# Kernel tuning notes

Measured on AMD Instinct MI355X. Metric: run time of the kernel, lower is better.

Reference implementation:

```python
import jax, jax.numpy as jnp
import numpy as np

B, V, C, H, W, D = 2, 3, 8, 128, 160, 64


def bilinear_sample(feat, grid):
    """feat: [B,C,H,W]; grid: [B,N,2] normalized to [-1,1], align_corners=True,
    padding_mode='zeros' (matches F.grid_sample). Returns [B,C,N]."""
    b, c, h, w = feat.shape
    ix = (grid[..., 0] + 1.0) * 0.5 * (w - 1)  # [B,N]
    iy = (grid[..., 1] + 1.0) * 0.5 * (h - 1)
    x0 = jnp.floor(ix)
    y0 = jnp.floor(iy)
    wx1 = ix - x0
    wy1 = iy - y0
    flat = feat.reshape(b, c, h * w)

    def corner(xi, yi, wgt):
        valid = (xi >= 0) & (xi <= w - 1) & (yi >= 0) & (yi <= h - 1)
        xc = jnp.clip(xi, 0, w - 1).astype(jnp.int32)
        yc = jnp.clip(yi, 0, h - 1).astype(jnp.int32)
        idx = yc * w + xc  # [B,N]
        vals = jnp.take_along_axis(flat, jnp.broadcast_to(idx[:, None, :], (b, c, idx.shape[1])), axis=2)
        return vals * (wgt * valid.astype(feat.dtype))[:, None, :]

    out = (corner(x0, y0, (1 - wx1) * (1 - wy1))
           + corner(x0 + 1, y0, wx1 * (1 - wy1))
           + corner(x0, y0 + 1, (1 - wx1) * wy1)
           + corner(x0 + 1, y0 + 1, wx1 * wy1))
    return out


def homo_warping(src_feat, proj_mat, depth_values):
    """src_feat [B,C,H,W], proj_mat [B,3,4], depth_values [B,D,H,W].
    Returns warped volume [B,C,D,H,W] and normalized grid [B,D,H,W,2]."""
    b, c, h, w = src_feat.shape
    d = depth_values.shape[1]
    R = proj_mat[:, :, :3]
    T = proj_mat[:, :, 3:]  # [B,3,1]
    ys, xs = jnp.meshgrid(jnp.arange(h, dtype=src_feat.dtype),
                          jnp.arange(w, dtype=src_feat.dtype), indexing='ij')
    ref = jnp.stack([xs.ravel(), ys.ravel(), jnp.ones(h * w, src_feat.dtype)], 0)  # [3,HW]
    Rp = jnp.einsum('bij,jp->bip', R, ref)  # [B,3,HW]
    dv = depth_values.reshape(b, d, h * w)
    src = Rp[:, :, None, :] + T[:, :, :, None] / dv[:, None, :, :]  # [B,3,D,HW]
    xy = src[:, :2] / src[:, 2:3]
    gx = xy[:, 0] / ((w - 1) / 2.0) - 1.0
    gy = xy[:, 1] / ((h - 1) / 2.0) - 1.0
    grid = jnp.stack([gx, gy], axis=-1)  # [B,D,HW,2]
    warped = bilinear_sample(src_feat, grid.reshape(b, d * h * w, 2)).reshape(b, c, d, h, w)
    return warped, grid.reshape(b, d, h, w, 2)


def setup_inputs() -> dict:
    key = jax.random.key(0)
    k1, k2, k3, k4, k5 = jax.random.split(key, 5)
    features = jax.random.normal(k1, (V, B, C, H, W), dtype=jnp.float32)
    # near-identity projective maps so warps land mostly in-bounds
    eye = jnp.broadcast_to(jnp.eye(3, dtype=jnp.float32), (B, V, 3, 3))
    Rm = eye + 0.01 * jax.random.normal(k2, (B, V, 3, 3), dtype=jnp.float32)
    Tm = 2.0 * jax.random.normal(k3, (B, V, 3, 1), dtype=jnp.float32)
    proj_matrices = jnp.concatenate([Rm, Tm], axis=-1)  # [B,V,3,4]
    base = jnp.linspace(2.0, 10.0, D, dtype=jnp.float32)[None, :, None, None]
    depth_values = base + 0.1 * jax.random.uniform(k4, (B, D, H, W), dtype=jnp.float32)
    reg_weight = jax.random.normal(k5, (C,), dtype=jnp.float32)
    return {"features": features, "proj_matrices": proj_matrices,
            "depth_values": depth_values, "reg_weight": reg_weight,
            "num_depth": D}


def reference(features, proj_matrices, depth_values, reg_weight, num_depth):
    v = features.shape[0]
    ref_feat = features[0]
    b, c, h, w = ref_feat.shape
    d = num_depth
    ref_volume = jnp.broadcast_to(ref_feat[:, :, None], (b, c, d, h, w))
    volume_sum = ref_volume
    volume_sq_sum = ref_volume ** 2
    in_masks = jnp.ones((b, 1, d, h, w), dtype=ref_feat.dtype)
    for i in range(1, v):  # fixed small number of source views
        warped, grid = homo_warping(features[i], proj_matrices[:, i], depth_values)
        m = (grid > -1.0) & (grid < 1.0)
        in_masks = in_masks + (m[..., 0] & m[..., 1]).astype(ref_feat.dtype)[:, None]
        volume_sum = volume_sum + warped
        volume_sq_sum = volume_sq_sum + warped ** 2
    count = 1.0 / in_masks
    volume_feat = volume_sq_sum * count - (volume_sum * count) ** 2  # [B,C,D,H,W]
    # stand-in cost regularization: channel reduction -> [B,D,H,W]
    cost = jnp.einsum('bcdhw,c->bdhw', volume_feat, reg_weight)
    prob_volume = jax.nn.softmax(cost, axis=1)
    depth = jnp.sum(prob_volume * depth_values, axis=1)  # [B,H,W]
    return depth
```

## Files before the change

### kernel.cpp

```cpp
#include <hip/hip_runtime.h>
#include <math.h>

#define BB 2
#define VV 3
#define CC 8
#define HH 128
#define WW 160
#define DD 64
constexpr int HW = HH * WW;
constexpr int NPIX = BB * HW;
constexpr int PX_PER_BLOCK = 16;
constexpr int CHUNKS = 16;
constexpr int DEPTHS_PER_CHUNK = DD / CHUNKS;

__global__ __launch_bounds__(256)
void transpose_feats(const float* __restrict__ feats, float* __restrict__ ft)
{
    const int t = blockIdx.x * blockDim.x + threadIdx.x;
    if (t >= VV * BB * HW) return;
    const int vb = t / HW;
    const int hw = t - vb * HW;
    const float* src = feats + (size_t)vb * CC * HW + hw;
    float* dst = ft + (size_t)vb * HW * CC + (size_t)hw * CC;
    float4 lo, hi;
    lo.x = src[0 * HW]; lo.y = src[1 * HW]; lo.z = src[2 * HW]; lo.w = src[3 * HW];
    hi.x = src[4 * HW]; hi.y = src[5 * HW]; hi.z = src[6 * HW]; hi.w = src[7 * HW];
    ((float4*)dst)[0] = lo;
    ((float4*)dst)[1] = hi;
}

__global__ __launch_bounds__(256)
void depthnet_fused(const float* __restrict__ ft,
                    const float* __restrict__ proj,
                    const float* __restrict__ depthv,
                    const float* __restrict__ regw,
                    float* __restrict__ out)
{
    __shared__ float sm_m[4 * PX_PER_BLOCK];
    __shared__ float sm_l[4 * PX_PER_BLOCK];
    __shared__ float sm_s[4 * PX_PER_BLOCK];

    const int tid   = threadIdx.x;
    const int lane  = tid & 63;
    const int wave  = tid >> 6;
    const int px    = lane & 15;
    const int sub   = lane >> 4;
    const int chunk = wave * 4 + sub;
    const int pixel = blockIdx.x * PX_PER_BLOCK + px;

    const int b  = (pixel >= HW) ? 1 : 0;
    const int hw = pixel - b * HW;
    const int h  = hw / WW;
    const int w  = hw - h * WW;

    const float* f0 = ft + ((size_t)b * HW + hw) * CC;
    float rf[CC], rf2[CC];
    {
        float4 lo = ((const float4*)f0)[0];
        float4 hi = ((const float4*)f0)[1];
        rf[0] = lo.x; rf[1] = lo.y; rf[2] = lo.z; rf[3] = lo.w;
        rf[4] = hi.x; rf[5] = hi.y; rf[6] = hi.z; rf[7] = hi.w;
    }
#pragma unroll
    for (int c = 0; c < CC; ++c) rf2[c] = rf[c] * rf[c];

    float Rp[2][3], Tv[2][3];
    const float xf = (float)w, yf = (float)h;
#pragma unroll
    for (int v = 0; v < 2; ++v) {
        const float* M = proj + ((size_t)b * VV + (v + 1)) * 12;
#pragma unroll
        for (int i = 0; i < 3; ++i) {
            Rp[v][i] = M[i * 4 + 0] * xf + M[i * 4 + 1] * yf + M[i * 4 + 2];
            Tv[v][i] = M[i * 4 + 3];
        }
    }

    const float* fsrc0 = ft + ((size_t)(1 * BB + b)) * HW * CC;
    const float* fsrc1 = ft + ((size_t)(2 * BB + b)) * HW * CC;

    float m = -INFINITY, l = 0.f, s = 0.f;

    const float* dvp = depthv + (size_t)b * DD * HW + hw;
    const int d0 = chunk * DEPTHS_PER_CHUNK;

    for (int dd = 0; dd < DEPTHS_PER_CHUNK; ++dd) {
        const int d = d0 + dd;
        const float dv = dvp[(size_t)d * HW];
        const float inv_dv = __builtin_amdgcn_rcpf(dv);

        float sum[CC], sq[CC];
#pragma unroll
        for (int c = 0; c < CC; ++c) { sum[c] = rf[c]; sq[c] = rf2[c]; }
        float nmask = 1.0f;

#pragma unroll
        for (int v = 0; v < 2; ++v) {
            const float* fb = (v == 0) ? fsrc0 : fsrc1;
            const float sx = Rp[v][0] + Tv[v][0] * inv_dv;
            const float sy = Rp[v][1] + Tv[v][1] * inv_dv;
            const float sz = Rp[v][2] + Tv[v][2] * inv_dv;
            const float rsz = __builtin_amdgcn_rcpf(sz);
            const float ix = sx * rsz;
            const float iy = sy * rsz;
            nmask += ((ix > 0.f) && (ix < (float)(WW - 1)) &&
                      (iy > 0.f) && (iy < (float)(HH - 1))) ? 1.0f : 0.0f;
            const float x0f = floorf(ix), y0f = floorf(iy);
            const float wx1 = ix - x0f, wy1 = iy - y0f;
            const float wx0 = 1.f - wx1, wy0 = 1.f - wy1;
            const float x1f = x0f + 1.f, y1f = y0f + 1.f;
            const bool vx0 = (x0f >= 0.f) && (x0f <= (float)(WW - 1));
            const bool vx1 = (x1f >= 0.f) && (x1f <= (float)(WW - 1));
            const bool vy0 = (y0f >= 0.f) && (y0f <= (float)(HH - 1));
            const bool vy1 = (y1f >= 0.f) && (y1f <= (float)(HH - 1));
            const float w00 = wx0 * wy0 * ((vx0 && vy0) ? 1.f : 0.f);
            const float w01 = wx1 * wy0 * ((vx1 && vy0) ? 1.f : 0.f);
            const float w10 = wx0 * wy1 * ((vx0 && vy1) ? 1.f : 0.f);
            const float w11 = wx1 * wy1 * ((vx1 && vy1) ? 1.f : 0.f);
            const int x0c = (int)fminf(fmaxf(x0f, 0.f), (float)(WW - 1));
            const int x1c = (int)fminf(fmaxf(x1f, 0.f), (float)(WW - 1));
            const int y0c = (int)fminf(fmaxf(y0f, 0.f), (float)(HH - 1));
            const int y1c = (int)fminf(fmaxf(y1f, 0.f), (float)(HH - 1));
            const int i00 = (y0c * WW + x0c) * CC;
            const int i01 = (y0c * WW + x1c) * CC;
            const int i10 = (y1c * WW + x0c) * CC;
            const int i11 = (y1c * WW + x1c) * CC;

            float val[CC];
            {
                float4 lo = *(const float4*)(fb + i00);
                float4 hi = *(const float4*)(fb + i00 + 4);
                val[0] = lo.x * w00; val[1] = lo.y * w00; val[2] = lo.z * w00; val[3] = lo.w * w00;
                val[4] = hi.x * w00; val[5] = hi.y * w00; val[6] = hi.z * w00; val[7] = hi.w * w00;
            }
            {
                float4 lo = *(const float4*)(fb + i01);
                float4 hi = *(const float4*)(fb + i01 + 4);
                val[0] += lo.x * w01; val[1] += lo.y * w01; val[2] += lo.z * w01; val[3] += lo.w * w01;
                val[4] += hi.x * w01; val[5] += hi.y * w01; val[6] += hi.z * w01; val[7] += hi.w * w01;
            }
            {
                float4 lo = *(const float4*)(fb + i10);
                float4 hi = *(const float4*)(fb + i10 + 4);
                val[0] += lo.x * w10; val[1] += lo.y * w10; val[2] += lo.z * w10; val[3] += lo.w * w10;
                val[4] += hi.x * w10; val[5] += hi.y * w10; val[6] += hi.z * w10; val[7] += hi.w * w10;
            }
            {
                float4 lo = *(const float4*)(fb + i11);
                float4 hi = *(const float4*)(fb + i11 + 4);
                val[0] += lo.x * w11; val[1] += lo.y * w11; val[2] += lo.z * w11; val[3] += lo.w * w11;
                val[4] += hi.x * w11; val[5] += hi.y * w11; val[6] += hi.z * w11; val[7] += hi.w * w11;
            }

#pragma unroll
            for (int c = 0; c < CC; ++c) {
                sum[c] += val[c];
                sq[c]  += val[c] * val[c];
            }
        }

        const float cnt = __builtin_amdgcn_rcpf(nmask);
        float t1 = 0.f, t2 = 0.f;
#pragma unroll
        for (int c = 0; c < CC; ++c) {
            t1 += regw[c] * sq[c];
            t2 += (regw[c] * sum[c]) * sum[c];
        }
        const float cost = cnt * t1 - (cnt * cnt) * t2;

        const float M = fmaxf(m, cost);
        const float e_old = __expf(m - M);
        const float e_new = __expf(cost - M);
        l = l * e_old + e_new;
        s = s * e_old + e_new * dv;
        m = M;
    }

#pragma unroll
    for (int off = 16; off < 64; off <<= 1) {
        const float m2 = __shfl_xor(m, off, 64);
        const float l2 = __shfl_xor(l, off, 64);
        const float s2 = __shfl_xor(s, off, 64);
        const float M  = fmaxf(m, m2);
        const float e1 = __expf(m - M);
        const float e2 = __expf(m2 - M);
        l = l * e1 + l2 * e2;
        s = s * e1 + s2 * e2;
        m = M;
    }

    if (lane < PX_PER_BLOCK) {
        sm_m[wave * PX_PER_BLOCK + px] = m;
        sm_l[wave * PX_PER_BLOCK + px] = l;
        sm_s[wave * PX_PER_BLOCK + px] = s;
    }
    __syncthreads();

    if (tid < PX_PER_BLOCK) {
        float M = sm_m[tid], L = sm_l[tid], S = sm_s[tid];
#pragma unroll
        for (int wv = 1; wv < 4; ++wv) {
            const float m2 = sm_m[wv * PX_PER_BLOCK + tid];
            const float l2 = sm_l[wv * PX_PER_BLOCK + tid];
            const float s2 = sm_s[wv * PX_PER_BLOCK + tid];
            const float Mn = fmaxf(M, m2);
            const float e1 = __expf(M - Mn);
            const float e2 = __expf(m2 - Mn);
            L = L * e1 + l2 * e2;
            S = S * e1 + s2 * e2;
            M = Mn;
        }
        out[blockIdx.x * PX_PER_BLOCK + tid] = S / L;
    }
}

extern "C" void kernel_launch(void* const* d_in, const int* in_sizes, int n_in,
                              void* d_out, int out_size, void* d_ws, size_t ws_size,
                              hipStream_t stream) {
    const float* feats  = (const float*)d_in[0];
    const float* proj   = (const float*)d_in[1];
    const float* depthv = (const float*)d_in[2];
    const float* regw   = (const float*)d_in[3];
    float* out = (float*)d_out;
    float* ft  = (float*)d_ws;

    {
        const int n = VV * BB * HW;
        const int block = 256;
        const int grid = (n + block - 1) / block;
        hipLaunchKernelGGL(transpose_feats, dim3(grid), dim3(block), 0, stream,
                           feats, ft);
    }
    {
        const int grid = NPIX / PX_PER_BLOCK;
        hipLaunchKernelGGL(depthnet_fused, dim3(grid), dim3(256), 0, stream,
                           ft, proj, depthv, regw, out);
    }
}
```

Measured before the change: 105.2 us.

## Transpose depth values, batch gather loads, and swizzle blocks across XCDs

Adds a kernel that transposes depth values to a pixel-major [B,HW,D] layout, so each thread reads its four depths with one float4 load instead of four strided loads. Hoists all 16 bilinear corner loads for both source views ahead of the arithmetic to raise memory-level parallelism. Remaps block indices so each XCD handles a contiguous pixel range, aiming for better L2 locality. The cost is an extra kernel launch, an extra full pass over the depth tensor, and more live registers.

```diff
diff --git a/kernel.cpp b/kernel.cpp
--- a/kernel.cpp
+++ b/kernel.cpp
@@ -12,6 +12,8 @@
 constexpr int PX_PER_BLOCK = 16;
 constexpr int CHUNKS = 16;
 constexpr int DEPTHS_PER_CHUNK = DD / CHUNKS;
+constexpr int GRID_FUSED = NPIX / PX_PER_BLOCK;
+constexpr int XCD_STRIDE = GRID_FUSED / 8;
 
 __global__ __launch_bounds__(256)
 void transpose_feats(const float* __restrict__ feats, float* __restrict__ ft)
@@ -30,9 +32,42 @@
 }
 
 __global__ __launch_bounds__(256)
+void transpose_dv(const float* __restrict__ dv, float* __restrict__ dvT)
+{
+    __shared__ float tile[64 * 65];
+    const int t   = threadIdx.x;
+    const int blk = blockIdx.x;
+    const int b   = blk / (HW / 64);
+    const int hw0 = (blk % (HW / 64)) * 64;
+
+    const float* src = dv + (size_t)b * DD * HW + hw0;
+    const int px = t & 63;
+    const int dq = t >> 6;
+#pragma unroll
+    for (int j = 0; j < 16; ++j) {
+        const int d = dq * 16 + j;
+        tile[px * 65 + d] = src[(size_t)d * HW + px];
+    }
+    __syncthreads();
+
+    float* dst = dvT + ((size_t)b * HW + hw0) * DD;
+    const int c = t & 15;
+#pragma unroll
+    for (int j = 0; j < 4; ++j) {
+        const int p = (t >> 4) + j * 16;
+        float4 v;
+        v.x = tile[p * 65 + c * 4 + 0];
+        v.y = tile[p * 65 + c * 4 + 1];
+        v.z = tile[p * 65 + c * 4 + 2];
+        v.w = tile[p * 65 + c * 4 + 3];
+        ((float4*)(dst + (size_t)p * DD))[c] = v;
+    }
+}
+
+__global__ __launch_bounds__(256)
 void depthnet_fused(const float* __restrict__ ft,
                     const float* __restrict__ proj,
-                    const float* __restrict__ depthv,
+                    const float* __restrict__ dvT,
                     const float* __restrict__ regw,
                     float* __restrict__ out)
 {
@@ -46,7 +81,8 @@
     const int px    = lane & 15;
     const int sub   = lane >> 4;
     const int chunk = wave * 4 + sub;
-    const int pixel = blockIdx.x * PX_PER_BLOCK + px;
+    const int bswz  = (blockIdx.x & 7) * XCD_STRIDE + (blockIdx.x >> 3);
+    const int pixel = bswz * PX_PER_BLOCK + px;
 
     const int b  = (pixel >= HW) ? 1 : 0;
     const int hw = pixel - b * HW;
@@ -79,24 +115,23 @@
     const float* fsrc0 = ft + ((size_t)(1 * BB + b)) * HW * CC;
     const float* fsrc1 = ft + ((size_t)(2 * BB + b)) * HW * CC;
 
+    const float4 dv4 = *(const float4*)(dvT + ((size_t)b * HW + hw) * DD + chunk * 4);
+    float dvv[4] = {dv4.x, dv4.y, dv4.z, dv4.w};
+    float inv[4];
+#pragma unroll
+    for (int k = 0; k < 4; ++k) inv[k] = __builtin_amdgcn_rcpf(dvv[k]);
+
     float m = -INFINITY, l = 0.f, s = 0.f;
 
-    const float* dvp = depthv + (size_t)b * DD * HW + hw;
-    const int d0 = chunk * DEPTHS_PER_CHUNK;
-
     for (int dd = 0; dd < DEPTHS_PER_CHUNK; ++dd) {
-        const int d = d0 + dd;
-        const float dv = dvp[(size_t)d * HW];
-        const float inv_dv = __builtin_amdgcn_rcpf(dv);
-
-        float sum[CC], sq[CC];
-#pragma unroll
-        for (int c = 0; c < CC; ++c) { sum[c] = rf[c]; sq[c] = rf2[c]; }
+        const float dv = dvv[dd];
+        const float inv_dv = inv[dd];
+
+        float wt[2][4];
+        int   ib[2][4];
         float nmask = 1.0f;
-
 #pragma unroll
         for (int v = 0; v < 2; ++v) {
-            const float* fb = (v == 0) ? fsrc0 : fsrc1;
             const float sx = Rp[v][0] + Tv[v][0] * inv_dv;
             const float sy = Rp[v][1] + Tv[v][1] * inv_dv;
             const float sz = Rp[v][2] + Tv[v][2] * inv_dv;
@@ -113,50 +148,63 @@
             const bool vx1 = (x1f >= 0.f) && (x1f <= (float)(WW - 1));
             const bool vy0 = (y0f >= 0.f) && (y0f <= (float)(HH - 1));
             const bool vy1 = (y1f >= 0.f) && (y1f <= (float)(HH - 1));
-            const float w00 = wx0 * wy0 * ((vx0 && vy0) ? 1.f : 0.f);
-            const float w01 = wx1 * wy0 * ((vx1 && vy0) ? 1.f : 0.f);
-            const float w10 = wx0 * wy1 * ((vx0 && vy1) ? 1.f : 0.f);
-            const float w11 = wx1 * wy1 * ((vx1 && vy1) ? 1.f : 0.f);
+            wt[v][0] = wx0 * wy0 * ((vx0 && vy0) ? 1.f : 0.f);
+            wt[v][1] = wx1 * wy0 * ((vx1 && vy0) ? 1.f : 0.f);
+            wt[v][2] = wx0 * wy1 * ((vx0 && vy1) ? 1.f : 0.f);
+            wt[v][3] = wx1 * wy1 * ((vx1 && vy1) ? 1.f : 0.f);
             const int x0c = (int)fminf(fmaxf(x0f, 0.f), (float)(WW - 1));
             const int x1c = (int)fminf(fmaxf(x1f, 0.f), (float)(WW - 1));
             const int y0c = (int)fminf(fmaxf(y0f, 0.f), (float)(HH - 1));
             const int y1c = (int)fminf(fmaxf(y1f, 0.f), (float)(HH - 1));
-            const int i00 = (y0c * WW + x0c) * CC;
-            const int i01 = (y0c * WW + x1c) * CC;
-            const int i10 = (y1c * WW + x0c) * CC;
-            const int i11 = (y1c * WW + x1c) * CC;
-
-            float val[CC];
-            {
-                float4 lo = *(const float4*)(fb + i00);
-                float4 hi = *(const float4*)(fb + i00 + 4);
-                val[0] = lo.x * w00; val[1] = lo.y * w00; val[2] = lo.z * w00; val[3] = lo.w * w00;
-                val[4] = hi.x * w00; val[5] = hi.y * w00; val[6] = hi.z * w00; val[7] = hi.w * w00;
-            }
-            {
-                float4 lo = *(const float4*)(fb + i01);
-                float4 hi = *(const float4*)(fb + i01 + 4);
-                val[0] += lo.x * w01; val[1] += lo.y * w01; val[2] += lo.z * w01; val[3] += lo.w * w01;
-                val[4] += hi.x * w01; val[5] += hi.y * w01; val[6] += hi.z * w01; val[7] += hi.w * w01;
-            }
-            {
-                float4 lo = *(const float4*)(fb + i10);
-                float4 hi = *(const float4*)(fb + i10 + 4);
-                val[0] += lo.x * w10; val[1] += lo.y * w10; val[2] += lo.z * w10; val[3] += lo.w * w10;
-                val[4] += hi.x * w10; val[5] += hi.y * w10; val[6] += hi.z * w10; val[7] += hi.w * w10;
-            }
-            {
-                float4 lo = *(const float4*)(fb + i11);
-                float4 hi = *(const float4*)(fb + i11 + 4);
-                val[0] += lo.x * w11; val[1] += lo.y * w11; val[2] += lo.z * w11; val[3] += lo.w * w11;
-                val[4] += hi.x * w11; val[5] += hi.y * w11; val[6] += hi.z * w11; val[7] += hi.w * w11;
-            }
-
-#pragma unroll
-            for (int c = 0; c < CC; ++c) {
-                sum[c] += val[c];
-                sq[c]  += val[c] * val[c];
-            }
+            ib[v][0] = (y0c * WW + x0c) * CC;
+            ib[v][1] = (y0c * WW + x1c) * CC;
+            ib[v][2] = (y1c * WW + x0c) * CC;
+            ib[v][3] = (y1c * WW + x1c) * CC;
+        }
+
+        float4 a0lo = *(const float4*)(fsrc0 + ib[0][0]);
+        float4 a0hi = *(const float4*)(fsrc0 + ib[0][0] + 4);
+        float4 a1lo = *(const float4*)(fsrc0 + ib[0][1]);
+        float4 a1hi = *(const float4*)(fsrc0 + ib[0][1] + 4);
+        float4 a2lo = *(const float4*)(fsrc0 + ib[0][2]);
+        float4 a2hi = *(const float4*)(fsrc0 + ib[0][2] + 4);
+        float4 a3lo = *(const float4*)(fsrc0 + ib[0][3]);
+        float4 a3hi = *(const float4*)(fsrc0 + ib[0][3] + 4);
+        float4 b0lo = *(const float4*)(fsrc1 + ib[1][0]);
+        float4 b0hi = *(const float4*)(fsrc1 + ib[1][0] + 4);
+        float4 b1lo = *(const float4*)(fsrc1 + ib[1][1]);
+        float4 b1hi = *(const float4*)(fsrc1 + ib[1][1] + 4);
+        float4 b2lo = *(const float4*)(fsrc1 + ib[1][2]);
+        float4 b2hi = *(const float4*)(fsrc1 + ib[1][2] + 4);
+        float4 b3lo = *(const float4*)(fsrc1 + ib[1][3]);
+        float4 b3hi = *(const float4*)(fsrc1 + ib[1][3] + 4);
+
+        float sum[CC], sq[CC];
+#pragma unroll
+        for (int c = 0; c < CC; ++c) { sum[c] = rf[c]; sq[c] = rf2[c]; }
+
+        float va[CC], vb[CC];
+        va[0] = a0lo.x * wt[0][0] + a1lo.x * wt[0][1] + a2lo.x * wt[0][2] + a3lo.x * wt[0][3];
+        va[1] = a0lo.y * wt[0][0] + a1lo.y * wt[0][1] + a2lo.y * wt[0][2] + a3lo.y * wt[0][3];
+        va[2] = a0lo.z * wt[0][0] + a1lo.z * wt[0][1] + a2lo.z * wt[0][2] + a3lo.z * wt[0][3];
+        va[3] = a0lo.w * wt[0][0] + a1lo.w * wt[0][1] + a2lo.w * wt[0][2] + a3lo.w * wt[0][3];
+        va[4] = a0hi.x * wt[0][0] + a1hi.x * wt[0][1] + a2hi.x * wt[0][2] + a3hi.x * wt[0][3];
+        va[5] = a0hi.y * wt[0][0] + a1hi.y * wt[0][1] + a2hi.y * wt[0][2] + a3hi.y * wt[0][3];
+        va[6] = a0hi.z * wt[0][0] + a1hi.z * wt[0][1] + a2hi.z * wt[0][2] + a3hi.z * wt[0][3];
+        va[7] = a0hi.w * wt[0][0] + a1hi.w * wt[0][1] + a2hi.w * wt[0][2] + a3hi.w * wt[0][3];
+        vb[0] = b0lo.x * wt[1][0] + b1lo.x * wt[1][1] + b2lo.x * wt[1][2] + b3lo.x * wt[1][3];
+        vb[1] = b0lo.y * wt[1][0] + b1lo.y * wt[1][1] + b2lo.y * wt[1][2] + b3lo.y * wt[1][3];
+        vb[2] = b0lo.z * wt[1][0] + b1lo.z * wt[1][1] + b2lo.z * wt[1][2] + b3lo.z * wt[1][3];
+        vb[3] = b0lo.w * wt[1][0] + b1lo.w * wt[1][1] + b2lo.w * wt[1][2] + b3lo.w * wt[1][3];
+        vb[4] = b0hi.x * wt[1][0] + b1hi.x * wt[1][1] + b2hi.x * wt[1][2] + b3hi.x * wt[1][3];
+        vb[5] = b0hi.y * wt[1][0] + b1hi.y * wt[1][1] + b2hi.y * wt[1][2] + b3hi.y * wt[1][3];
+        vb[6] = b0hi.z * wt[1][0] + b1hi.z * wt[1][1] + b2hi.z * wt[1][2] + b3hi.z * wt[1][3];
+        vb[7] = b0hi.w * wt[1][0] + b1hi.w * wt[1][1] + b2hi.w * wt[1][2] + b3hi.w * wt[1][3];
+
+#pragma unroll
+        for (int c = 0; c < CC; ++c) {
+            sum[c] += va[c] + vb[c];
+            sq[c]  += va[c] * va[c] + vb[c] * vb[c];
         }
 
         const float cnt = __builtin_amdgcn_rcpf(nmask);
@@ -210,7 +258,7 @@
             S = S * e1 + s2 * e2;
             M = Mn;
         }
-        out[blockIdx.x * PX_PER_BLOCK + tid] = S / L;
+        out[bswz * PX_PER_BLOCK + tid] = S / L;
     }
 }
 
@@ -223,17 +271,20 @@
     const float* regw   = (const float*)d_in[3];
     float* out = (float*)d_out;
     float* ft  = (float*)d_ws;
+    float* dvT = (float*)d_ws + (size_t)VV * BB * HW * CC;
 
     {
         const int n = VV * BB * HW;
-        const int block = 256;
-        const int grid = (n + block - 1) / block;
-        hipLaunchKernelGGL(transpose_feats, dim3(grid), dim3(block), 0, stream,
+        hipLaunchKernelGGL(transpose_feats, dim3((n + 255) / 256), dim3(256), 0, stream,
                            feats, ft);
     }
     {
-        const int grid = NPIX / PX_PER_BLOCK;
-        hipLaunchKernelGGL(depthnet_fused, dim3(grid), dim3(256), 0, stream,
-                           ft, proj, depthv, regw, out);
-    }
-}
+        const int grid = BB * (HW / 64);
+        hipLaunchKernelGGL(transpose_dv, dim3(grid), dim3(256), 0, stream,
+                           depthv, dvT);
+    }
+    {
+        hipLaunchKernelGGL(depthnet_fused, dim3(GRID_FUSED), dim3(256), 0, stream,
+                           ft, proj, dvT, regw, out);
+    }
+}
```

Measured after the change: 113.3 us. +7.7%, slower.
